# Kernel optimization log

Measured on AMD Instinct MI355X. Metric: run time of the kernel, lower is better.

## Reference

```python
import jax, jax.numpy as jnp
import numpy as np

EPS = 1e-08
SIGMA = 0.1
B = 1.0


def setup_inputs() -> dict:
    key = jax.random.key(0)
    k1, k2 = jax.random.split(key)
    N, C, H, W = 4, 256, 64, 64
    featureT = jax.random.normal(k1, (N, C, H, W), dtype=jnp.float32)
    featureI = jax.random.normal(k2, (N, C, H, W), dtype=jnp.float32)
    return {"featureT": featureT, "featureI": featureI}


def reference(featureT, featureI):
    N, C, H, W = featureT.shape
    # center both by target mean over (batch, spatial)
    meanT = featureT.mean(axis=(0, 2, 3), keepdims=True)
    fI = featureI - meanT
    fT = featureT - meanT
    # channel-wise L2 normalize
    fI = fI / (jnp.linalg.norm(fI, axis=1, keepdims=True) + EPS)
    fT = fT / (jnp.linalg.norm(fT, axis=1, keepdims=True) + EPS)
    # 1x1-patch conv2d == contraction over channels: sim[n, p, h, w]
    # where p indexes the flattened H*W spatial positions of the target.
    fT_flat = fT.reshape(N, C, H * W)  # [N, C, P]
    sim = jnp.einsum('nchw,ncp->nphw', fI, fT_flat)  # [N, P, H, W]
    raw_dist = (1.0 - sim) / 2.0
    # relative distances: divide by min over patch axis
    div = jnp.min(raw_dist, axis=1, keepdims=True)
    relative_dist = raw_dist / (div + EPS)
    # contextual similarity: exp-weight + sum-normalize over patch axis
    Wt = jnp.exp((B - relative_dist) / (SIGMA + EPS))
    W_sum = Wt.sum(axis=1, keepdims=True)
    CX = Wt / (W_sum + EPS)
    # max over spatial dims of featureI, mean over patches, -log, mean over batch
    CX = CX.max(axis=(2, 3))           # [N, P]
    CX = CX.mean(axis=1)               # [N]
    CX_loss = -jnp.log(CX + EPS)
    return jnp.mean(CX_loss)
```

## Files before the change

### kernel.cpp

```cpp
#include <hip/hip_runtime.h>
#include <cmath>


#define NB 4
#define CC 256
#define HW 4096
#define NQ0 8
#define NP1 32

static constexpr float kEPS = 1e-8f;
static constexpr float kSIG = 0.1f + 1e-8f;

typedef __attribute__((ext_vector_type(8)))  short short8;
typedef __attribute__((ext_vector_type(16))) float f32x16;

enum {
  OFF_MEAN = 0,
  OFF_CMAX = 256,
  OFF_WSUM = OFF_CMAX + NQ0*NB*HW,
  OFF_MAXV = OFF_WSUM + NP1*NB*HW,
  OFF_GB   = OFF_MAXV + NB*HW,
  OFF_GT   = OFF_GB + 2*NB*HW,
  OFF_GI   = OFF_GT + NB*HW*CC/2,
  OFF_S    = OFF_GI + NB*HW*CC/2,
  WS_FLOATS_FULL = OFF_S + NB*HW*HW/2
};

__device__ __forceinline__ ushort cvt_bf16(float x) {
  unsigned u = __float_as_uint(x);
  unsigned r = (u + 0x7fffu + ((u >> 16) & 1u)) >> 16;
  return (ushort)r;
}
__device__ __forceinline__ float bf2f(ushort u) {
  return __uint_as_float((unsigned)u << 16);
}

__device__ __forceinline__ float blockSum256(float v) {
  __shared__ float sh[4];
  const int lane = threadIdx.x & 63, wv = threadIdx.x >> 6;
  #pragma unroll
  for (int o = 32; o > 0; o >>= 1) v += __shfl_down(v, o, 64);
  __syncthreads();
  if (lane == 0) sh[wv] = v;
  __syncthreads();
  return sh[0] + sh[1] + sh[2] + sh[3];
}

__global__ __launch_bounds__(256) void k_mean9(const float* __restrict__ fT,
                                               float* __restrict__ ws) {
  const int c = blockIdx.x, t = threadIdx.x;
  float s = 0.f;
  for (int n = 0; n < NB; ++n) {
    const float* p = fT + (size_t)(n*CC + c)*HW;
    #pragma unroll
    for (int k = 0; k < 16; ++k) s += p[k*256 + t];
  }
  const float tot = blockSum256(s);
  if (t == 0) ws[OFF_MEAN + c] = tot * (1.0f/16384.0f);
}

__global__ __launch_bounds__(256) void k_prep9(const float* __restrict__ fT,
                                               const float* __restrict__ fI,
                                               float* __restrict__ ws) {
  __shared__ float stage[32][257];
  __shared__ float prt[8][32];
  __shared__ float sinv[32];
  const int t = threadIdx.x, l = t & 63;
  int bid = blockIdx.x;
  const int tensor = (bid >= 512); bid &= 511;
  const int n   = bid >> 7;
  const int r32 = bid & 127;
  const int p0  = r32 * 32;

  const float* __restrict__ src = tensor ? fI : fT;
  ushort* __restrict__ dst = (ushort*)(ws + (tensor ? OFF_GI : OFF_GT));
  const float* __restrict__ mean = ws + OFF_MEAN;

  const int pl = t & 31, cg = t >> 5;
  float acc = 0.f;
  #pragma unroll
  for (int i = 0; i < 32; ++i) {
    const int c = cg*32 + i;
    const float v = src[((size_t)(n*CC + c))*HW + p0 + pl] - mean[c];
    stage[pl][c] = v;
    acc += v*v;
  }
  prt[cg][pl] = acc;
  __syncthreads();
  if (t < 32) {
    float s = 0.f;
    #pragma unroll
    for (int g = 0; g < 8; ++g) s += prt[g][t];
    sinv[t] = 1.0f/(sqrtf(s) + kEPS);
  }
  __syncthreads();

  const int w = t >> 6, lhi = l >> 5, m = l & 31;
  const float iv = sinv[m];
  #pragma unroll
  for (int i = 0; i < 4; ++i) {
    const int kc = w*4 + i;
    const int cb = kc*16 + lhi*8;
    short8 o;
    #pragma unroll
    for (int j = 0; j < 8; ++j)
      ((ushort*)&o)[j] = cvt_bf16(stage[m][cb + j] * iv);
    *(short8*)(dst + (((size_t)(n*128 + r32)*16 + kc) << 9) + l*8) = o;
  }
}

__global__ __launch_bounds__(256, 4) void k_gemm9(
    const ushort* __restrict__ gA, const ushort* __restrict__ gB,
    float* __restrict__ ws)
{
  __shared__ ushort Ab[2][8192];
  __shared__ float red2[128];

  const int t = threadIdx.x;
  const int w = t >> 6, l = t & 63;
  const int ln31 = l & 31, lhi = l >> 5;

  const int b = blockIdx.x;
  const int h = b & 7, sid = b >> 3;
  const int n = sid >> 5;
  const int col0 = (sid & 31) * 128;

  const ushort* __restrict__ gAn = gA + (size_t)(n*128 + h*16)*8192;

  short8 pf[4];
  #pragma unroll
  for (int i = 0; i < 4; ++i)
    pf[i] = *(const short8*)(gAn + (size_t)(i*256 + t)*8);
  #pragma unroll
  for (int i = 0; i < 4; ++i)
    *(short8*)&Ab[0][(i*256 + t)*8] = pf[i];
  #pragma unroll
  for (int i = 0; i < 4; ++i)
    pf[i] = *(const short8*)(gAn + 8192 + (size_t)(i*256 + t)*8);

  const int RB = (col0 >> 5) + w;
  short8 breg[16];
  #pragma unroll
  for (int kc = 0; kc < 16; ++kc)
    breg[kc] = *(const short8*)(gB +
        (((size_t)(n*128 + RB)*16 + kc) << 9) + l*8);

  const int qc = col0 + w*32 + ln31;
  ushort* __restrict__ Sq = (ushort*)(ws + OFF_S) + (size_t)n*HW*HW + qc;

  float runl = -3.0e38f;

  for (int iter = 0; iter < 16; ++iter) {
    const int p = iter & 1;
    __syncthreads();
    if (iter + 1 < 16) {
      #pragma unroll
      for (int i = 0; i < 4; ++i)
        *(short8*)&Ab[p^1][(i*256 + t)*8] = pf[i];
      if (iter + 2 < 16) {
        const ushort* __restrict__ src = gAn + (size_t)(iter + 2)*8192;
        #pragma unroll
        for (int i = 0; i < 4; ++i)
          pf[i] = *(const short8*)(src + (size_t)(i*256 + t)*8);
      }
    }

    f32x16 acc;
    #pragma unroll
    for (int e = 0; e < 16; ++e) acc[e] = 0.f;
    #pragma unroll
    for (int kc = 0; kc < 16; ++kc) {
      const short8 a0 = *(const short8*)&Ab[p][kc*512 + l*8];
      acc = __builtin_amdgcn_mfma_f32_32x32x16_bf16(a0, breg[kc], acc, 0, 0, 0);
    }

    const int pb = h*512 + iter*32 + 4*lhi;
    #pragma unroll
    for (int r = 0; r < 16; ++r) {
      const int prow = pb + (r & 3) + 8*(r >> 2);
      const ushort u = cvt_bf16(acc[r]);
      Sq[(size_t)prow * HW] = u;
      runl = fmaxf(runl, bf2f(u));
    }
  }

  {
    const float o = __shfl_xor(runl, 32, 64);
    runl = fmaxf(runl, o);
  }
  if (l < 32) red2[w*32 + ln31] = runl;
  __syncthreads();
  if (t < 128)
    ws[OFF_CMAX + h*(NB*HW) + n*HW + col0 + t] = red2[t];
}

__global__ __launch_bounds__(256) void k_pass1(float* __restrict__ ws) {
  const int t = threadIdx.x;
  const int b = blockIdx.x;
  const int pc = b & 31, rest = b >> 5;
  const int n = rest >> 3, qblk = rest & 7;
  const int q = qblk*512 + 2*t;

  float a0, b0, a1, b1;
  {
    float cm0 = -3.0e38f, cm1 = -3.0e38f;
    #pragma unroll
    for (int hh = 0; hh < NQ0; ++hh) {
      cm0 = fmaxf(cm0, ws[OFF_CMAX + hh*(NB*HW) + n*HW + q]);
      cm1 = fmaxf(cm1, ws[OFF_CMAX + hh*(NB*HW) + n*HW + q + 1]);
    }
    const float i0 = 1.0f/(2.0f*(0.5f*(1.0f - cm0) + kEPS));
    const float i1 = 1.0f/(2.0f*(0.5f*(1.0f - cm1) + kEPS));
    b0 = i0 / kSIG; a0 = (1.0f - i0) / kSIG;
    b1 = i1 / kSIG; a1 = (1.0f - i1) / kSIG;
  }

  const ushort* __restrict__ S =
      (const ushort*)(ws + OFF_S) + (size_t)n*HW*HW + q;
  float acc0 = 0.f, acc1 = 0.f;
  const int p0 = pc*128;
  #pragma unroll 8
  for (int i = 0; i < 128; ++i) {
    const ushort2 u = *(const ushort2*)(S + (size_t)(p0 + i)*HW);
    acc0 += __expf(fmaf(b0, bf2f(u.x), a0));
    acc1 += __expf(fmaf(b1, bf2f(u.y), a1));
  }
  float2 o; o.x = acc0; o.y = acc1;
  *(float2*)&ws[OFF_WSUM + pc*(NB*HW) + n*HW + q] = o;
}

__global__ __launch_bounds__(256) void k_gb9(float* __restrict__ ws) {
  const int idx = blockIdx.x*256 + threadIdx.x;
  float cm = -3.0e38f;
  #pragma unroll
  for (int hh = 0; hh < NQ0; ++hh)
    cm = fmaxf(cm, ws[OFF_CMAX + hh*(NB*HW) + idx]);
  const float inv2d = 1.0f/(2.0f*(0.5f*(1.0f - cm) + kEPS));
  const float beta  = inv2d / kSIG;
  const float alpha = (1.0f - inv2d) / kSIG;
  float sw = 0.f;
  #pragma unroll
  for (int pc = 0; pc < NP1; ++pc)
    sw += ws[OFF_WSUM + pc*(NB*HW) + idx];
  ws[OFF_GB + idx]         = alpha - logf(sw + kEPS);
  ws[OFF_GB + NB*HW + idx] = beta;
}

__global__ __launch_bounds__(256) void k_pass2(float* __restrict__ ws) {
  __shared__ float gq[4096], bq[4096];
  const int t = threadIdx.x, w = t >> 6, l = t & 63;
  const int b = blockIdx.x;
  const int n = b >> 8, pg = b & 255;

  const float* __restrict__ G  = ws + OFF_GB + n*HW;
  const float* __restrict__ Bq = ws + OFF_GB + NB*HW + n*HW;
  #pragma unroll
  for (int i = 0; i < 4; ++i) {
    *(float4*)&gq[(i*256 + t)*4] = *(const float4*)&G [(i*256 + t)*4];
    *(float4*)&bq[(i*256 + t)*4] = *(const float4*)&Bq[(i*256 + t)*4];
  }
  __syncthreads();

  const ushort* __restrict__ S =
      (const ushort*)(ws + OFF_S) + (size_t)n*HW*HW;
  #pragma unroll
  for (int r = 0; r < 4; ++r) {
    const int p = pg*16 + w*4 + r;
    const ushort* __restrict__ row = S + (size_t)p*HW;
    float m = -3.0e38f;
    #pragma unroll 4
    for (int it = 0; it < 32; ++it) {
      const int q = it*128 + 2*l;
      const ushort2 u = *(const ushort2*)(row + q);
      m = fmaxf(m, fmaf(bq[q],     bf2f(u.x), gq[q]));
      m = fmaxf(m, fmaf(bq[q + 1], bf2f(u.y), gq[q + 1]));
    }
    #pragma unroll
    for (int o = 32; o > 0; o >>= 1) m = fmaxf(m, __shfl_xor(m, o, 64));
    if (l == 0) ws[OFF_MAXV + n*HW + p] = m;
  }
}

__global__ __launch_bounds__(256) void k_final9(const float* __restrict__ ws,
                                                float* __restrict__ out) {
  const int t = threadIdx.x;
  float loss = 0.f;
  for (int n = 0; n < NB; ++n) {
    float s = 0.f;
    for (int k = 0; k < 16; ++k)
      s += __expf(ws[OFF_MAXV + n*HW + k*256 + t]);
    const float tot = blockSum256(s);
    loss += -logf(tot*(1.0f/4096.0f) + kEPS);
  }
  if (t == 0) out[0] = loss*0.25f;
}

extern "C" void kernel_launch(void* const* d_in, const int* in_sizes, int n_in,
                              void* d_out, int out_size, void* d_ws, size_t ws_size,
                              hipStream_t stream) {
  const float* fT = (const float*)d_in[0];
  const float* fI = (const float*)d_in[1];
  float* out = (float*)d_out;
  float* ws  = (float*)d_ws;

  const size_t need_full = (size_t)WS_FLOATS_FULL * sizeof(float);
  if (ws_size < need_full) return;

  const ushort* GT = (const ushort*)(ws + OFF_GT);
  const ushort* GI = (const ushort*)(ws + OFF_GI);
  k_mean9 <<<256,  256, 0, stream>>>(fT, ws);
  k_prep9 <<<1024, 256, 0, stream>>>(fT, fI, ws);
  k_gemm9 <<<1024, 256, 0, stream>>>(GT, GI, ws);
  k_pass1 <<<1024, 256, 0, stream>>>(ws);
  k_gb9   <<<64,   256, 0, stream>>>(ws);
  k_pass2 <<<1024, 256, 0, stream>>>(ws);
  k_final9<<<1,    256, 0, stream>>>(ws, out);
}
```

Before: 205.6 us.

## Stage GEMM output tile through LDS for coalesced 16-byte global stores

The bf16 similarity results, previously written straight to global memory as scattered 2-byte stores, are now staged in a padded LDS tile. Each row is then written back with 16-byte vector stores, which should make the global writes of the large S matrix coalesced. To free LDS, the A operand moves from a double buffer to a single buffer with register prefetch of one iteration ahead. This adds extra __syncthreads per iteration and weakens the overlap between loads and compute.

```diff
diff --git a/kernel.cpp b/kernel.cpp
--- a/kernel.cpp
+++ b/kernel.cpp
@@ -113,7 +113,8 @@
     const ushort* __restrict__ gA, const ushort* __restrict__ gB,
     float* __restrict__ ws)
 {
-  __shared__ ushort Ab[2][8192];
+  __shared__ ushort Ab[8192];
+  __shared__ ushort Eb[32*136];
   __shared__ float red2[128];
 
   const int t = threadIdx.x;
@@ -131,12 +132,6 @@
   #pragma unroll
   for (int i = 0; i < 4; ++i)
     pf[i] = *(const short8*)(gAn + (size_t)(i*256 + t)*8);
-  #pragma unroll
-  for (int i = 0; i < 4; ++i)
-    *(short8*)&Ab[0][(i*256 + t)*8] = pf[i];
-  #pragma unroll
-  for (int i = 0; i < 4; ++i)
-    pf[i] = *(const short8*)(gAn + 8192 + (size_t)(i*256 + t)*8);
 
   const int RB = (col0 >> 5) + w;
   short8 breg[16];
@@ -145,42 +140,51 @@
     breg[kc] = *(const short8*)(gB +
         (((size_t)(n*128 + RB)*16 + kc) << 9) + l*8);
 
-  const int qc = col0 + w*32 + ln31;
-  ushort* __restrict__ Sq = (ushort*)(ws + OFF_S) + (size_t)n*HW*HW + qc;
+  ushort* __restrict__ Sn = (ushort*)(ws + OFF_S) + (size_t)n*HW*HW;
+
+  const int ecol = w*32 + ln31;
+  const int rrow = t >> 4;
+  const int rq   = (t & 15) * 8;
 
   float runl = -3.0e38f;
 
   for (int iter = 0; iter < 16; ++iter) {
-    const int p = iter & 1;
     __syncthreads();
+    #pragma unroll
+    for (int i = 0; i < 4; ++i)
+      *(short8*)&Ab[(i*256 + t)*8] = pf[i];
     if (iter + 1 < 16) {
+      const ushort* __restrict__ src = gAn + (size_t)(iter + 1)*8192;
       #pragma unroll
       for (int i = 0; i < 4; ++i)
-        *(short8*)&Ab[p^1][(i*256 + t)*8] = pf[i];
-      if (iter + 2 < 16) {
-        const ushort* __restrict__ src = gAn + (size_t)(iter + 2)*8192;
-        #pragma unroll
-        for (int i = 0; i < 4; ++i)
-          pf[i] = *(const short8*)(src + (size_t)(i*256 + t)*8);
-      }
-    }
+        pf[i] = *(const short8*)(src + (size_t)(i*256 + t)*8);
+    }
+    __syncthreads();
 
     f32x16 acc;
     #pragma unroll
     for (int e = 0; e < 16; ++e) acc[e] = 0.f;
     #pragma unroll
     for (int kc = 0; kc < 16; ++kc) {
-      const short8 a0 = *(const short8*)&Ab[p][kc*512 + l*8];
+      const short8 a0 = *(const short8*)&Ab[kc*512 + l*8];
       acc = __builtin_amdgcn_mfma_f32_32x32x16_bf16(a0, breg[kc], acc, 0, 0, 0);
     }
 
-    const int pb = h*512 + iter*32 + 4*lhi;
     #pragma unroll
     for (int r = 0; r < 16; ++r) {
-      const int prow = pb + (r & 3) + 8*(r >> 2);
+      const int lrow = 4*lhi + (r & 3) + 8*(r >> 2);
       const ushort u = cvt_bf16(acc[r]);
-      Sq[(size_t)prow * HW] = u;
+      Eb[lrow*136 + ecol] = u;
       runl = fmaxf(runl, bf2f(u));
+    }
+    __syncthreads();
+
+    const int pb = h*512 + iter*32;
+    #pragma unroll
+    for (int k = 0; k < 2; ++k) {
+      const int lr = rrow + 16*k;
+      const short8 v = *(const short8*)&Eb[lr*136 + rq];
+      *(short8*)(Sn + (size_t)(pb + lr)*HW + col0 + rq) = v;
     }
   }
 
```

After: 176.5 us. 14.2% less time.
